# Performance work log

Measured on AMD Instinct MI355X. Metric: run time of the kernel, lower is better.

Reference implementation:

```python
import jax, jax.numpy as jnp
import numpy as np

_EPS = 1e-5
RC = 5.0   # cutoff radius
L = 20     # number of radial basis functions
N = 10000  # nodes
E = 100000 # edges
F = 128    # in_feats


def _ssp(x):
    # ShiftedSoftplus: softplus(x) - log(2)
    return jax.nn.softplus(x) - jnp.log(2.0)


def _rbf(r):
    # DimeNet radial basis: sqrt(2/rc) * sin(n*pi*r/rc) / r, n = 1..L.  r: [E,1] -> [E,L]
    n = jnp.arange(1, L + 1, dtype=r.dtype)
    return jnp.sqrt(2.0 / RC) * jnp.sin(n * jnp.pi * r / RC) / r


def _fc(u):
    # cosine cutoff applied elementwise: 0.5*(cos(pi*u/rc)+1) for u < rc else 0
    return jnp.where(u < RC, 0.5 * (jnp.cos(jnp.pi * u / RC) + 1.0), 0.0)


def setup_inputs() -> dict:
    key = jax.random.key(0)
    ks = jax.random.split(key, 12)

    def nrm(k, shape, scale=1.0):
        return jax.random.normal(k, shape, dtype=jnp.float32) * scale

    return {
        "x": nrm(ks[0], (N, 3)) * 3.0,           # atomic positions
        "v": nrm(ks[1], (N, F, 3)),               # vector node features
        "s": nrm(ks[2], (N, F)),                  # scalar node features
        "ms1_w": nrm(ks[3], (F, F), F ** -0.5),
        "ms1_b": jnp.zeros((F,), jnp.float32),
        "ms2_w": nrm(ks[4], (3 * F, F), F ** -0.5),
        "ms2_b": jnp.zeros((3 * F,), jnp.float32),
        "mv_w": nrm(ks[5], (3 * F, L), L ** -0.5),
        "mv_b": jnp.zeros((3 * F,), jnp.float32),
        "us1_w": nrm(ks[6], (F, F), F ** -0.5),
        "us1_b": jnp.zeros((F,), jnp.float32),
        "us2_w": nrm(ks[7], (3 * F, F), F ** -0.5),
        "us2_b": jnp.zeros((3 * F,), jnp.float32),
        "src": jax.random.randint(ks[8], (E,), 0, N, dtype=jnp.int32),
        "dst": jax.random.randint(ks[9], (E,), 0, N, dtype=jnp.int32),
    }


def reference(x, v, s, ms1_w, ms1_b, ms2_w, ms2_b, mv_w, mv_b,
              us1_w, us1_b, us2_w, us2_b, src, dst):
    # ---------- pass 1: message1 + reduce1 (sum over incoming edges) ----------
    sj = s[src]                                   # [E,F]   src scalar features
    vj = v[src]                                   # [E,F,3] src vector features
    vec = x[src] - x[dst]                         # [E,3]   x_i - x_j (molecule branch)
    r = jnp.sqrt(jnp.sum(vec ** 2, axis=-1) + _EPS)[:, None]          # [E,1]
    phi = _ssp(sj @ ms1_w.T + ms1_b) @ ms2_w.T + ms2_b                 # [E,3F]
    w = _fc(_rbf(r) @ mv_w.T + mv_b)                                    # [E,3F]
    v_, s_, r_ = jnp.split(phi * w, 3, axis=-1)                         # each [E,F]
    dv_e = vj * v_[:, :, None] + r_[:, :, None] * (vec / r)[:, None, :] # [E,F,3]
    dv = jax.ops.segment_sum(dv_e, dst, num_segments=N)                 # [N,F,3]
    ds = jax.ops.segment_sum(s_, dst, num_segments=N)                   # [N,F]
    v_new = v + dv
    s_new = s + ds

    # ---------- pass 2: message2 + reduce2 (mean over incoming edges) ----------
    s2 = _ssp(s_new[src] @ us1_w.T + us1_b) @ us2_w.T + us2_b           # [E,3F]
    deg = jax.ops.segment_sum(jnp.ones((E,), s.dtype), dst, num_segments=N)
    denom = jnp.maximum(deg, 1.0)
    s_mean = jax.ops.segment_sum(s2, dst, num_segments=N) / denom[:, None]        # [N,3F]
    uv = jax.ops.segment_sum(v_new[src], dst, num_segments=N) / denom[:, None, None]  # [N,F,3]
    avv, asv, ass = jnp.split(s_mean, 3, axis=-1)                       # each [N,F]
    norm = jnp.sqrt(jnp.sum(uv ** 2, axis=-1) + _EPS)[..., None]        # [N,F,1]
    dv2 = uv * avv[:, :, None]                                           # [N,F,3]
    ds2 = jnp.sum((uv / norm) ** 2, axis=-1) * asv + ass                 # [N,F]
    return (v_new + dv2, s_new + ds2)
```

## Files before the change

### kernel.cpp

```cpp
#include <hip/hip_runtime.h>
#include <hip/hip_bf16.h>


#define F_DIM   128
#define F3_DIM  384
#define L_DIM   20
#define CAP     64
#define BATCH   16

typedef __attribute__((ext_vector_type(8))) short short8;
typedef __attribute__((ext_vector_type(4))) float f32x4;
typedef __attribute__((ext_vector_type(4))) unsigned short us4;

struct u3 { unsigned a, b, c; };

__device__ __forceinline__ unsigned short f2bf(float f) {
  union { float f; unsigned u; } a; a.f = f;
  unsigned u = a.u;
  u = (u + 0x7FFFu + ((u >> 16) & 1u)) >> 16;
  return (unsigned short)u;
}
__device__ __forceinline__ float bf2f(unsigned short u) {
  union { unsigned u; float f; } a; a.u = ((unsigned)u) << 16;
  return a.f;
}

__global__ __launch_bounds__(256) void cast_fill_kernel(
    const float* __restrict__ ms1_w, unsigned short* __restrict__ w_ms1,
    const float* __restrict__ ms2_w, unsigned short* __restrict__ w_ms2,
    const float* __restrict__ us1_w, unsigned short* __restrict__ w_us1,
    const float* __restrict__ us2_w, unsigned short* __restrict__ w_us2,
    const float* __restrict__ s,     unsigned short* __restrict__ sbf,
    const float* __restrict__ v,     us4* __restrict__ v4,
    const float* __restrict__ mv_w,  unsigned short* __restrict__ mvwB,
    const int* __restrict__ src, const int* __restrict__ dst,
    int* __restrict__ cursor, int* __restrict__ jbuf,
    int nF, int E)
{
  int i = blockIdx.x * 256 + threadIdx.x;
  if (i < 16384) w_ms1[i] = f2bf(ms1_w[i]);
  if (i < 49152) w_ms2[i] = f2bf(ms2_w[i]);
  if (i < 16384) w_us1[i] = f2bf(us1_w[i]);
  if (i < 49152) w_us2[i] = f2bf(us2_w[i]);
  if (i < nF)    sbf[i] = f2bf(s[i]);
  if (i < nF) {
    const float* vp = v + (size_t)i * 3;
    us4 o; o.x = f2bf(vp[0]); o.y = f2bf(vp[1]); o.z = f2bf(vp[2]); o.w = 0;
    v4[i] = o;
  }
  if (i < 384 * 32) {
    int o = i >> 5, k = i & 31;
    float val = (k < 20) ? mv_w[o * 20 + k] * 0.6324555320336759f : 0.f;
    mvwB[i] = f2bf(val);
  }
  if (i < E) {
    int d = dst[i];
    int p = atomicAdd(&cursor[d], 1);
    if (p < CAP) jbuf[d * CAP + p] = src[i];
  }
}

__global__ __launch_bounds__(64) void mlp_kernel(
    const unsigned short* __restrict__ X,
    const unsigned short* __restrict__ W1,
    const float* __restrict__ B1,
    const unsigned short* __restrict__ W2,
    const float* __restrict__ B2,
    const us4* __restrict__ Vin,
    unsigned short* __restrict__ Yc)
{
  __shared__ float HT[128 * 17];
  const int lane = threadIdx.x;
  const int c    = lane & 15;
  const int quad = lane >> 4;
  const int m0   = blockIdx.x * 16;

  f32x4 acc[8];
#pragma unroll
  for (int t = 0; t < 8; t++) acc[t] = (f32x4){0.f, 0.f, 0.f, 0.f};
#pragma unroll
  for (int kk = 0; kk < 4; kk++) {
    short8 a = *(const short8*)(X + (size_t)(m0 + c) * 128 + kk * 32 + quad * 8);
#pragma unroll
    for (int t = 0; t < 8; t++) {
      short8 b = *(const short8*)(W1 + (size_t)(t * 16 + c) * 128 + kk * 32 + quad * 8);
      acc[t] = __builtin_amdgcn_mfma_f32_16x16x32_bf16(a, b, acc[t], 0, 0, 0);
    }
  }
#pragma unroll
  for (int t = 0; t < 8; t++) {
    float bias = B1[t * 16 + c];
    int k = t * 16 + c;
#pragma unroll
    for (int r = 0; r < 4; r++) {
      float h = acc[t][r] + bias;
      float sp = (h > 15.f) ? h : log1pf(__expf(h));
      sp -= 0.69314718056f;
      HT[k * 17 + quad * 4 + r] = sp;
    }
  }
  __syncthreads();

  f32x4 acc2[3][8];
#pragma unroll
  for (int g = 0; g < 3; g++)
#pragma unroll
    for (int t = 0; t < 8; t++) acc2[g][t] = (f32x4){0.f, 0.f, 0.f, 0.f};
#pragma unroll
  for (int kk = 0; kk < 4; kk++) {
    short8 afr;
#pragma unroll
    for (int j = 0; j < 8; j++) {
      float hv = HT[(kk * 32 + quad * 8 + j) * 17 + c];
      afr[j] = (short)f2bf(hv);
    }
#pragma unroll
    for (int g = 0; g < 3; g++)
#pragma unroll
      for (int t = 0; t < 8; t++) {
        short8 b = *(const short8*)(W2 + (size_t)(g * 128 + t * 16 + c) * 128 + kk * 32 + quad * 8);
        acc2[g][t] = __builtin_amdgcn_mfma_f32_16x16x32_bf16(afr, b, acc2[g][t], 0, 0, 0);
      }
  }
#pragma unroll
  for (int t = 0; t < 8; t++) {
    int f = t * 16 + c;
    float b0 = B2[f], b1 = B2[128 + f], b2 = B2[256 + f];
#pragma unroll
    for (int r = 0; r < 4; r++) {
      int m = quad * 4 + r;
      us4 vv = Vin[(size_t)(m0 + m) * 128 + f];
      unsigned p0 = f2bf(acc2[0][t][r] + b0);
      unsigned p1 = f2bf(acc2[1][t][r] + b1);
      unsigned p2 = f2bf(acc2[2][t][r] + b2);
      u3 rec;
      rec.a = p0 | (p1 << 16);
      rec.b = p2 | ((unsigned)vv.x << 16);
      rec.c = (unsigned)vv.y | ((unsigned)vv.z << 16);
      *(u3*)(Yc + ((size_t)(m0 + m) * 128 + f) * 6) = rec;
    }
  }
}

__global__ __launch_bounds__(256, 4) void pass1_kernel(
    const float* __restrict__ x,
    const unsigned short* __restrict__ combo1,
    const float* __restrict__ v,
    const float* __restrict__ s,
    const unsigned short* __restrict__ mvwB,
    const float* __restrict__ mv_b,
    const int* __restrict__ jbuf,
    const int* __restrict__ deg,
    float* __restrict__ vnew, us4* __restrict__ vnew4,
    float* __restrict__ snew, unsigned short* __restrict__ snew_bf, int nNodes)
{
  __shared__ unsigned short Asn[BATCH * 32];
  __shared__ float4 Au[BATCH];
  __shared__ us4 Wl[BATCH * 128];
  __shared__ float red[512];

  const int tid  = threadIdx.x;
  const int wave = tid >> 6, lane = tid & 63;
  const int half = wave >> 1, split = wave & 1;
  const int i = blockIdx.x;
  const int f = lane + 64 * half;
  const int c = lane & 15, quad = lane >> 4;

  int cnt = deg[i]; if (cnt > CAP) cnt = CAP;
  const int base = i * CAP;

  short8 bfr[6]; float bias[6];
#pragma unroll
  for (int p = 0; p < 3; p++)
#pragma unroll
    for (int h = 0; h < 2; h++) {
      int t = 2 * wave + h + 8 * p;
      bfr[p * 2 + h]  = *(const short8*)(mvwB + (size_t)(t * 16 + c) * 32 + quad * 8);
      bias[p * 2 + h] = mv_b[t * 16 + c];
    }

  const float xi0 = x[i * 3], xi1 = x[i * 3 + 1], xi2 = x[i * 3 + 2];
  int jv = (lane < cnt) ? jbuf[base + lane] : 0;

  float accV0 = 0.f, accV1 = 0.f, accV2 = 0.f, accS = 0.f;

  for (int bs = 0; bs < cnt; bs += BATCH) {
    int bcnt = cnt - bs; if (bcnt > BATCH) bcnt = BATCH;
    __syncthreads();

    if (wave == 0) {
      int t16 = lane & (BATCH - 1);
      int e = bs + t16;
      int j = __shfl(jv, e);
      if (lane < BATCH && e < cnt) {
        float d0 = x[j * 3]     - xi0;
        float d1 = x[j * 3 + 1] - xi1;
        float d2 = x[j * 3 + 2] - xi2;
        float r = sqrtf(d0 * d0 + d1 * d1 + d2 * d2 + 1e-5f);
        float invr = 1.0f / r;
        Au[lane] = make_float4(d0 * invr, d1 * invr, d2 * invr, invr);
        float theta = r * 0.6283185307179586f;
        float s1, c1;
        __sincosf(theta, &s1, &c1);
        float c2 = 2.f * c1;
        float pm2 = s1, pm1 = c2 * s1;
        Asn[lane * 32 + 0] = f2bf(pm2);
        Asn[lane * 32 + 1] = f2bf(pm1);
#pragma unroll
        for (int l = 2; l < L_DIM; l++) {
          float cur = c2 * pm1 - pm2;
          Asn[lane * 32 + l] = f2bf(cur);
          pm2 = pm1; pm1 = cur;
        }
#pragma unroll
        for (int l = L_DIM; l < 32; l++) Asn[lane * 32 + l] = 0;
      }
    }
    __syncthreads();

    {
      short8 a = *(const short8*)&Asn[c * 32 + quad * 8];
      f32x4 acc[6];
#pragma unroll
      for (int q = 0; q < 6; q++)
        acc[q] = __builtin_amdgcn_mfma_f32_16x16x32_bf16(
            a, bfr[q], (f32x4){0.f, 0.f, 0.f, 0.f}, 0, 0, 0);
#pragma unroll
      for (int r = 0; r < 4; r++) {
        int el = quad * 4 + r;
        if (el < bcnt) {
          float invr = Au[el].w;
#pragma unroll
          for (int h = 0; h < 2; h++) {
            float wp0 = fmaf(acc[h][r],     invr, bias[h]);
            float wp1 = fmaf(acc[2 + h][r], invr, bias[2 + h]);
            float wp2 = fmaf(acc[4 + h][r], invr, bias[4 + h]);
            float w0 = (wp0 < 5.f) ? 0.5f * (__cosf(wp0 * 0.6283185307179586f) + 1.f) : 0.f;
            float w1 = (wp1 < 5.f) ? 0.5f * (__cosf(wp1 * 0.6283185307179586f) + 1.f) : 0.f;
            float w2 = (wp2 < 5.f) ? 0.5f * (__cosf(wp2 * 0.6283185307179586f) + 1.f) : 0.f;
            us4 o; o.x = f2bf(w0); o.y = f2bf(w1); o.z = f2bf(w2); o.w = 0;
            Wl[el * 128 + wave * 32 + h * 16 + c] = o;
          }
        }
      }
    }
    __syncthreads();

    u3 cb[8];
    float msk[8];
#pragma unroll
    for (int k = 0; k < 8; k++) {
      int e = split + 2 * k;
      int ec = (e < bcnt) ? e : 0;
      msk[k] = (e < bcnt) ? 1.f : 0.f;
      int j = __shfl(jv, bs + ec);
      cb[k] = *(const u3*)(combo1 + ((size_t)j * 128 + f) * 6);
    }
#pragma unroll
    for (int k = 0; k < 8; k++) {
      int e = split + 2 * k;
      int ec = (e < bcnt) ? e : 0;
      float4 u = Au[ec];
      us4 wv = Wl[ec * 128 + f];
      float ph0 = bf2f((unsigned short)(cb[k].a & 0xffff));
      float ph1 = bf2f((unsigned short)(cb[k].a >> 16));
      float ph2 = bf2f((unsigned short)(cb[k].b & 0xffff));
      float vx  = bf2f((unsigned short)(cb[k].b >> 16));
      float vy  = bf2f((unsigned short)(cb[k].c & 0xffff));
      float vz  = bf2f((unsigned short)(cb[k].c >> 16));
      float m0 = ph0 * bf2f(wv.x) * msk[k];
      float m1 = ph1 * bf2f(wv.y) * msk[k];
      float m2 = ph2 * bf2f(wv.z) * msk[k];
      accV0 = fmaf(vx, m0, fmaf(m2, u.x, accV0));
      accV1 = fmaf(vy, m0, fmaf(m2, u.y, accV1));
      accV2 = fmaf(vz, m0, fmaf(m2, u.z, accV2));
      accS += m1;
    }
  }

  const int idx = half * 64 + lane;
  __syncthreads();
  if (split == 1) {
    red[idx * 4 + 0] = accV0; red[idx * 4 + 1] = accV1;
    red[idx * 4 + 2] = accV2; red[idx * 4 + 3] = accS;
  }
  __syncthreads();
  if (split == 0) {
    accV0 += red[idx * 4 + 0]; accV1 += red[idx * 4 + 1];
    accV2 += red[idx * 4 + 2]; accS  += red[idx * 4 + 3];
    size_t b3 = (size_t)i * 384 + f * 3;
    float n0 = v[b3] + accV0, n1 = v[b3 + 1] + accV1, n2 = v[b3 + 2] + accV2;
    vnew[b3] = n0; vnew[b3 + 1] = n1; vnew[b3 + 2] = n2;
    us4 o; o.x = f2bf(n0); o.y = f2bf(n1); o.z = f2bf(n2); o.w = 0;
    vnew4[(size_t)i * 128 + f] = o;
    size_t b1 = (size_t)i * 128 + f;
    float sv = s[b1] + accS;
    snew[b1] = sv;
    snew_bf[b1] = f2bf(sv);
  }
}

__global__ __launch_bounds__(256, 4) void pass2_kernel(
    const float* __restrict__ vnew,
    const float* __restrict__ snew,
    const unsigned short* __restrict__ combo2,
    const int* __restrict__ jbuf, const int* __restrict__ deg,
    float* __restrict__ vout, float* __restrict__ sout, int nNodes)
{
  __shared__ float red[1024];
  const int wave = threadIdx.x >> 6, lane = threadIdx.x & 63;
  const int half = wave >> 1, split = wave & 1;
  const int i = blockIdx.x;
  const int f = lane + 64 * half;

  int cnt = deg[i]; if (cnt > CAP) cnt = CAP;
  const int base = i * CAP;
  int jv = (lane < cnt) ? jbuf[base + lane] : 0;

  float accU0 = 0.f, accU1 = 0.f, accU2 = 0.f;
  float accM0 = 0.f, accM1 = 0.f, accM2 = 0.f;

  for (int b0 = split; b0 < cnt; b0 += 16) {
    u3 cb[8];
    float msk[8];
#pragma unroll
    for (int k = 0; k < 8; k++) {
      int e = b0 + 2 * k;
      int ec = (e < cnt) ? e : 0;
      msk[k] = (e < cnt) ? 1.f : 0.f;
      int j = __shfl(jv, ec);
      cb[k] = *(const u3*)(combo2 + ((size_t)j * 128 + f) * 6);
    }
#pragma unroll
    for (int k = 0; k < 8; k++) {
      accM0 = fmaf(bf2f((unsigned short)(cb[k].a & 0xffff)), msk[k], accM0);
      accM1 = fmaf(bf2f((unsigned short)(cb[k].a >> 16)),    msk[k], accM1);
      accM2 = fmaf(bf2f((unsigned short)(cb[k].b & 0xffff)), msk[k], accM2);
      accU0 = fmaf(bf2f((unsigned short)(cb[k].b >> 16)),    msk[k], accU0);
      accU1 = fmaf(bf2f((unsigned short)(cb[k].c & 0xffff)), msk[k], accU1);
      accU2 = fmaf(bf2f((unsigned short)(cb[k].c >> 16)),    msk[k], accU2);
    }
  }

  const int idx = half * 64 + lane;
  if (split == 1) {
    red[idx * 8 + 0] = accU0; red[idx * 8 + 1] = accU1; red[idx * 8 + 2] = accU2;
    red[idx * 8 + 3] = accM0; red[idx * 8 + 4] = accM1; red[idx * 8 + 5] = accM2;
  }
  __syncthreads();
  if (split == 0) {
    accU0 += red[idx * 8 + 0]; accU1 += red[idx * 8 + 1]; accU2 += red[idx * 8 + 2];
    accM0 += red[idx * 8 + 3]; accM1 += red[idx * 8 + 4]; accM2 += red[idx * 8 + 5];

    float dinv = 1.0f / (float)(cnt > 0 ? cnt : 1);
    float uv0 = accU0 * dinv, uv1 = accU1 * dinv, uv2 = accU2 * dinv;
    float avv = accM0 * dinv, asv = accM1 * dinv, ass = accM2 * dinv;
    float q = uv0 * uv0 + uv1 * uv1 + uv2 * uv2;
    float ds2 = (q / (q + 1e-5f)) * asv + ass;
    size_t b3 = (size_t)i * 384 + f * 3;
    vout[b3]     = vnew[b3]     + uv0 * avv;
    vout[b3 + 1] = vnew[b3 + 1] + uv1 * avv;
    vout[b3 + 2] = vnew[b3 + 2] + uv2 * avv;
    size_t b1 = (size_t)i * 128 + f;
    sout[b1] = snew[b1] + ds2;
  }
}

extern "C" void kernel_launch(void* const* d_in, const int* in_sizes, int n_in,
                              void* d_out, int out_size, void* d_ws, size_t ws_size,
                              hipStream_t stream)
{
  const float* x     = (const float*)d_in[0];
  const float* v     = (const float*)d_in[1];
  const float* s     = (const float*)d_in[2];
  const float* ms1_w = (const float*)d_in[3];
  const float* ms1_b = (const float*)d_in[4];
  const float* ms2_w = (const float*)d_in[5];
  const float* ms2_b = (const float*)d_in[6];
  const float* mv_w  = (const float*)d_in[7];
  const float* mv_b  = (const float*)d_in[8];
  const float* us1_w = (const float*)d_in[9];
  const float* us1_b = (const float*)d_in[10];
  const float* us2_w = (const float*)d_in[11];
  const float* us2_b = (const float*)d_in[12];
  const int*   src   = (const int*)d_in[13];
  const int*   dst   = (const int*)d_in[14];

  const int N = in_sizes[0] / 3;
  const int E = in_sizes[13];

  char* p = (char*)d_ws;
  auto alloc = [&](size_t bytes) -> void* {
    void* r = (void*)p;
    p += (bytes + 255) & ~(size_t)255;
    return r;
  };
  unsigned short* sbf   = (unsigned short*)alloc((size_t)N * 128 * 2);
  unsigned short* snbf  = (unsigned short*)alloc((size_t)N * 128 * 2);
  unsigned short* w_ms1 = (unsigned short*)alloc(16384 * 2);
  unsigned short* w_ms2 = (unsigned short*)alloc(49152 * 2);
  unsigned short* w_us1 = (unsigned short*)alloc(16384 * 2);
  unsigned short* w_us2 = (unsigned short*)alloc(49152 * 2);
  unsigned short* mvwB  = (unsigned short*)alloc(384 * 32 * 2);
  us4*   v4     = (us4*)alloc((size_t)N * 128 * 8);
  us4*   vnew4  = (us4*)alloc((size_t)N * 128 * 8);
  unsigned short* combo1 = (unsigned short*)alloc((size_t)N * 128 * 12);
  unsigned short* combo2 = (unsigned short*)alloc((size_t)N * 128 * 12);
  float* vnew   = (float*)alloc((size_t)N * 384 * 4);
  float* snew   = (float*)alloc((size_t)N * 128 * 4);
  int* cursor   = (int*)alloc((size_t)N * 4);
  int* jbuf     = (int*)alloc((size_t)N * CAP * 4);

  hipMemsetAsync(cursor, 0, (size_t)N * 4, stream);

  cast_fill_kernel<<<(N * 128 + 255) / 256, 256, 0, stream>>>(
      ms1_w, w_ms1, ms2_w, w_ms2, us1_w, w_us1, us2_w, w_us2,
      s, sbf, v, v4, mv_w, mvwB, src, dst, cursor, jbuf, N * 128, E);

  mlp_kernel<<<N / 16, 64, 0, stream>>>(sbf, w_ms1, ms1_b, w_ms2, ms2_b,
                                        v4, combo1);

  pass1_kernel<<<N, 256, 0, stream>>>(x, combo1, v, s, mvwB, mv_b,
                                      jbuf, cursor, vnew, vnew4, snew, snbf, N);

  mlp_kernel<<<N / 16, 64, 0, stream>>>(snbf, w_us1, us1_b, w_us2, us2_b,
                                        vnew4, combo2);

  float* vout = (float*)d_out;
  float* sout = vout + (size_t)N * 384;
  pass2_kernel<<<N, 256, 0, stream>>>(vnew, snew, combo2, jbuf, cursor,
                                      vout, sout, N);
}
```

Before: 244.1 us.

## Split MLP tiles across 8 waves and replace edge masks with zero sentinel row

```diff
diff --git a/kernel.cpp b/kernel.cpp
--- a/kernel.cpp
+++ b/kernel.cpp
@@ -35,6 +35,7 @@
     const float* __restrict__ mv_w,  unsigned short* __restrict__ mvwB,
     const int* __restrict__ src, const int* __restrict__ dst,
     int* __restrict__ cursor, int* __restrict__ jbuf,
+    unsigned short* __restrict__ c1pad, unsigned short* __restrict__ c2pad,
     int nF, int E)
 {
   int i = blockIdx.x * 256 + threadIdx.x;
@@ -53,6 +54,10 @@
     float val = (k < 20) ? mv_w[o * 20 + k] * 0.6324555320336759f : 0.f;
     mvwB[i] = f2bf(val);
   }
+  if (i < 768) {
+    c1pad[i] = 0;
+    c2pad[i] = 0;
+  }
   if (i < E) {
     int d = dst[i];
     int p = atomicAdd(&cursor[d], 1);
@@ -60,7 +65,7 @@
   }
 }
 
-__global__ __launch_bounds__(64) void mlp_kernel(
+__global__ __launch_bounds__(512) void mlp_kernel(
     const unsigned short* __restrict__ X,
     const unsigned short* __restrict__ W1,
     const float* __restrict__ B1,
@@ -70,30 +75,25 @@
     unsigned short* __restrict__ Yc)
 {
   __shared__ float HT[128 * 17];
-  const int lane = threadIdx.x;
+  const int lane = threadIdx.x & 63;
+  const int wave = threadIdx.x >> 6;
   const int c    = lane & 15;
   const int quad = lane >> 4;
   const int m0   = blockIdx.x * 16;
 
-  f32x4 acc[8];
-#pragma unroll
-  for (int t = 0; t < 8; t++) acc[t] = (f32x4){0.f, 0.f, 0.f, 0.f};
+  f32x4 acc = (f32x4){0.f, 0.f, 0.f, 0.f};
 #pragma unroll
   for (int kk = 0; kk < 4; kk++) {
     short8 a = *(const short8*)(X + (size_t)(m0 + c) * 128 + kk * 32 + quad * 8);
-#pragma unroll
-    for (int t = 0; t < 8; t++) {
-      short8 b = *(const short8*)(W1 + (size_t)(t * 16 + c) * 128 + kk * 32 + quad * 8);
-      acc[t] = __builtin_amdgcn_mfma_f32_16x16x32_bf16(a, b, acc[t], 0, 0, 0);
-    }
-  }
-#pragma unroll
-  for (int t = 0; t < 8; t++) {
-    float bias = B1[t * 16 + c];
-    int k = t * 16 + c;
+    short8 b = *(const short8*)(W1 + (size_t)(wave * 16 + c) * 128 + kk * 32 + quad * 8);
+    acc = __builtin_amdgcn_mfma_f32_16x16x32_bf16(a, b, acc, 0, 0, 0);
+  }
+  {
+    int k = wave * 16 + c;
+    float bias = B1[k];
 #pragma unroll
     for (int r = 0; r < 4; r++) {
-      float h = acc[t][r] + bias;
+      float h = acc[r] + bias;
       float sp = (h > 15.f) ? h : log1pf(__expf(h));
       sp -= 0.69314718056f;
       HT[k * 17 + quad * 4 + r] = sp;
@@ -101,11 +101,9 @@
   }
   __syncthreads();
 
-  f32x4 acc2[3][8];
-#pragma unroll
-  for (int g = 0; g < 3; g++)
-#pragma unroll
-    for (int t = 0; t < 8; t++) acc2[g][t] = (f32x4){0.f, 0.f, 0.f, 0.f};
+  f32x4 acc2[3];
+#pragma unroll
+  for (int g = 0; g < 3; g++) acc2[g] = (f32x4){0.f, 0.f, 0.f, 0.f};
 #pragma unroll
   for (int kk = 0; kk < 4; kk++) {
     short8 afr;
@@ -115,24 +113,21 @@
       afr[j] = (short)f2bf(hv);
     }
 #pragma unroll
-    for (int g = 0; g < 3; g++)
-#pragma unroll
-      for (int t = 0; t < 8; t++) {
-        short8 b = *(const short8*)(W2 + (size_t)(g * 128 + t * 16 + c) * 128 + kk * 32 + quad * 8);
-        acc2[g][t] = __builtin_amdgcn_mfma_f32_16x16x32_bf16(afr, b, acc2[g][t], 0, 0, 0);
-      }
-  }
-#pragma unroll
-  for (int t = 0; t < 8; t++) {
-    int f = t * 16 + c;
+    for (int g = 0; g < 3; g++) {
+      short8 b = *(const short8*)(W2 + (size_t)(g * 128 + wave * 16 + c) * 128 + kk * 32 + quad * 8);
+      acc2[g] = __builtin_amdgcn_mfma_f32_16x16x32_bf16(afr, b, acc2[g], 0, 0, 0);
+    }
+  }
+  {
+    int f = wave * 16 + c;
     float b0 = B2[f], b1 = B2[128 + f], b2 = B2[256 + f];
 #pragma unroll
     for (int r = 0; r < 4; r++) {
       int m = quad * 4 + r;
       us4 vv = Vin[(size_t)(m0 + m) * 128 + f];
-      unsigned p0 = f2bf(acc2[0][t][r] + b0);
-      unsigned p1 = f2bf(acc2[1][t][r] + b1);
-      unsigned p2 = f2bf(acc2[2][t][r] + b2);
+      unsigned p0 = f2bf(acc2[0][r] + b0);
+      unsigned p1 = f2bf(acc2[1][r] + b1);
+      unsigned p2 = f2bf(acc2[2][r] + b2);
       u3 rec;
       rec.a = p0 | (p1 << 16);
       rec.b = p2 | ((unsigned)vv.x << 16);
@@ -180,7 +175,7 @@
     }
 
   const float xi0 = x[i * 3], xi1 = x[i * 3 + 1], xi2 = x[i * 3 + 2];
-  int jv = (lane < cnt) ? jbuf[base + lane] : 0;
+  int jv = (lane < cnt) ? jbuf[base + lane] : nNodes;
 
   float accV0 = 0.f, accV1 = 0.f, accV2 = 0.f, accS = 0.f;
 
@@ -192,28 +187,34 @@
       int t16 = lane & (BATCH - 1);
       int e = bs + t16;
       int j = __shfl(jv, e);
-      if (lane < BATCH && e < cnt) {
-        float d0 = x[j * 3]     - xi0;
-        float d1 = x[j * 3 + 1] - xi1;
-        float d2 = x[j * 3 + 2] - xi2;
-        float r = sqrtf(d0 * d0 + d1 * d1 + d2 * d2 + 1e-5f);
-        float invr = 1.0f / r;
-        Au[lane] = make_float4(d0 * invr, d1 * invr, d2 * invr, invr);
-        float theta = r * 0.6283185307179586f;
-        float s1, c1;
-        __sincosf(theta, &s1, &c1);
-        float c2 = 2.f * c1;
-        float pm2 = s1, pm1 = c2 * s1;
-        Asn[lane * 32 + 0] = f2bf(pm2);
-        Asn[lane * 32 + 1] = f2bf(pm1);
-#pragma unroll
-        for (int l = 2; l < L_DIM; l++) {
-          float cur = c2 * pm1 - pm2;
-          Asn[lane * 32 + l] = f2bf(cur);
-          pm2 = pm1; pm1 = cur;
+      if (lane < BATCH) {
+        if (e < cnt) {
+          float d0 = x[j * 3]     - xi0;
+          float d1 = x[j * 3 + 1] - xi1;
+          float d2 = x[j * 3 + 2] - xi2;
+          float r = sqrtf(d0 * d0 + d1 * d1 + d2 * d2 + 1e-5f);
+          float invr = 1.0f / r;
+          Au[lane] = make_float4(d0 * invr, d1 * invr, d2 * invr, invr);
+          float theta = r * 0.6283185307179586f;
+          float s1, c1;
+          __sincosf(theta, &s1, &c1);
+          float c2 = 2.f * c1;
+          float pm2 = s1, pm1 = c2 * s1;
+          Asn[lane * 32 + 0] = f2bf(pm2);
+          Asn[lane * 32 + 1] = f2bf(pm1);
+#pragma unroll
+          for (int l = 2; l < L_DIM; l++) {
+            float cur = c2 * pm1 - pm2;
+            Asn[lane * 32 + l] = f2bf(cur);
+            pm2 = pm1; pm1 = cur;
+          }
+#pragma unroll
+          for (int l = L_DIM; l < 32; l++) Asn[lane * 32 + l] = 0;
+        } else {
+          Au[lane] = make_float4(0.f, 0.f, 0.f, 0.f);
+#pragma unroll
+          for (int l = 0; l < 32; l++) Asn[lane * 32 + l] = 0;
         }
-#pragma unroll
-        for (int l = L_DIM; l < 32; l++) Asn[lane * 32 + l] = 0;
       }
     }
     __syncthreads();
@@ -241,36 +242,35 @@
             us4 o; o.x = f2bf(w0); o.y = f2bf(w1); o.z = f2bf(w2); o.w = 0;
             Wl[el * 128 + wave * 32 + h * 16 + c] = o;
           }
+        } else {
+          us4 z; z.x = 0; z.y = 0; z.z = 0; z.w = 0;
+          Wl[el * 128 + wave * 32 + c]      = z;
+          Wl[el * 128 + wave * 32 + 16 + c] = z;
         }
       }
     }
     __syncthreads();
 
     u3 cb[8];
-    float msk[8];
 #pragma unroll
     for (int k = 0; k < 8; k++) {
-      int e = split + 2 * k;
-      int ec = (e < bcnt) ? e : 0;
-      msk[k] = (e < bcnt) ? 1.f : 0.f;
-      int j = __shfl(jv, bs + ec);
+      int j = __shfl(jv, bs + split + 2 * k);
       cb[k] = *(const u3*)(combo1 + ((size_t)j * 128 + f) * 6);
     }
 #pragma unroll
     for (int k = 0; k < 8; k++) {
-      int e = split + 2 * k;
-      int ec = (e < bcnt) ? e : 0;
-      float4 u = Au[ec];
-      us4 wv = Wl[ec * 128 + f];
+      int el = split + 2 * k;
+      float4 u = Au[el];
+      us4 wv = Wl[el * 128 + f];
       float ph0 = bf2f((unsigned short)(cb[k].a & 0xffff));
       float ph1 = bf2f((unsigned short)(cb[k].a >> 16));
       float ph2 = bf2f((unsigned short)(cb[k].b & 0xffff));
       float vx  = bf2f((unsigned short)(cb[k].b >> 16));
       float vy  = bf2f((unsigned short)(cb[k].c & 0xffff));
       float vz  = bf2f((unsigned short)(cb[k].c >> 16));
-      float m0 = ph0 * bf2f(wv.x) * msk[k];
-      float m1 = ph1 * bf2f(wv.y) * msk[k];
-      float m2 = ph2 * bf2f(wv.z) * msk[k];
+      float m0 = ph0 * bf2f(wv.x);
+      float m1 = ph1 * bf2f(wv.y);
+      float m2 = ph2 * bf2f(wv.z);
       accV0 = fmaf(vx, m0, fmaf(m2, u.x, accV0));
       accV1 = fmaf(vy, m0, fmaf(m2, u.y, accV1));
       accV2 = fmaf(vz, m0, fmaf(m2, u.z, accV2));
@@ -315,30 +315,28 @@
 
   int cnt = deg[i]; if (cnt > CAP) cnt = CAP;
   const int base = i * CAP;
-  int jv = (lane < cnt) ? jbuf[base + lane] : 0;
+  int jv = (lane < cnt) ? jbuf[base + lane] : nNodes;
 
   float accU0 = 0.f, accU1 = 0.f, accU2 = 0.f;
   float accM0 = 0.f, accM1 = 0.f, accM2 = 0.f;
 
   for (int b0 = split; b0 < cnt; b0 += 16) {
     u3 cb[8];
-    float msk[8];
 #pragma unroll
     for (int k = 0; k < 8; k++) {
       int e = b0 + 2 * k;
-      int ec = (e < cnt) ? e : 0;
-      msk[k] = (e < cnt) ? 1.f : 0.f;
+      int ec = (e < 63) ? e : 63;
       int j = __shfl(jv, ec);
       cb[k] = *(const u3*)(combo2 + ((size_t)j * 128 + f) * 6);
     }
 #pragma unroll
     for (int k = 0; k < 8; k++) {
-      accM0 = fmaf(bf2f((unsigned short)(cb[k].a & 0xffff)), msk[k], accM0);
-      accM1 = fmaf(bf2f((unsigned short)(cb[k].a >> 16)),    msk[k], accM1);
-      accM2 = fmaf(bf2f((unsigned short)(cb[k].b & 0xffff)), msk[k], accM2);
-      accU0 = fmaf(bf2f((unsigned short)(cb[k].b >> 16)),    msk[k], accU0);
-      accU1 = fmaf(bf2f((unsigned short)(cb[k].c & 0xffff)), msk[k], accU1);
-      accU2 = fmaf(bf2f((unsigned short)(cb[k].c >> 16)),    msk[k], accU2);
+      accM0 += bf2f((unsigned short)(cb[k].a & 0xffff));
+      accM1 += bf2f((unsigned short)(cb[k].a >> 16));
+      accM2 += bf2f((unsigned short)(cb[k].b & 0xffff));
+      accU0 += bf2f((unsigned short)(cb[k].b >> 16));
+      accU1 += bf2f((unsigned short)(cb[k].c & 0xffff));
+      accU2 += bf2f((unsigned short)(cb[k].c >> 16));
     }
   }
 
@@ -404,8 +402,8 @@
   unsigned short* mvwB  = (unsigned short*)alloc(384 * 32 * 2);
   us4*   v4     = (us4*)alloc((size_t)N * 128 * 8);
   us4*   vnew4  = (us4*)alloc((size_t)N * 128 * 8);
-  unsigned short* combo1 = (unsigned short*)alloc((size_t)N * 128 * 12);
-  unsigned short* combo2 = (unsigned short*)alloc((size_t)N * 128 * 12);
+  unsigned short* combo1 = (unsigned short*)alloc((size_t)(N + 1) * 128 * 12);
+  unsigned short* combo2 = (unsigned short*)alloc((size_t)(N + 1) * 128 * 12);
   float* vnew   = (float*)alloc((size_t)N * 384 * 4);
   float* snew   = (float*)alloc((size_t)N * 128 * 4);
   int* cursor   = (int*)alloc((size_t)N * 4);
@@ -415,16 +413,17 @@
 
   cast_fill_kernel<<<(N * 128 + 255) / 256, 256, 0, stream>>>(
       ms1_w, w_ms1, ms2_w, w_ms2, us1_w, w_us1, us2_w, w_us2,
-      s, sbf, v, v4, mv_w, mvwB, src, dst, cursor, jbuf, N * 128, E);
-
-  mlp_kernel<<<N / 16, 64, 0, stream>>>(sbf, w_ms1, ms1_b, w_ms2, ms2_b,
-                                        v4, combo1);
+      s, sbf, v, v4, mv_w, mvwB, src, dst, cursor, jbuf,
+      combo1 + (size_t)N * 768, combo2 + (size_t)N * 768, N * 128, E);
+
+  mlp_kernel<<<N / 16, 512, 0, stream>>>(sbf, w_ms1, ms1_b, w_ms2, ms2_b,
+                                         v4, combo1);
 
   pass1_kernel<<<N, 256, 0, stream>>>(x, combo1, v, s, mvwB, mv_b,
                                       jbuf, cursor, vnew, vnew4, snew, snbf, N);
 
-  mlp_kernel<<<N / 16, 64, 0, stream>>>(snbf, w_us1, us1_b, w_us2, us2_b,
-                                        vnew4, combo2);
+  mlp_kernel<<<N / 16, 512, 0, stream>>>(snbf, w_us1, us1_b, w_us2, us2_b,
+                                         vnew4, combo2);
 
   float* vout = (float*)d_out;
   float* sout = vout + (size_t)N * 384;
```

Result: faster. 224.9 us (-7.9%).
